# Performance work log

Measured on AMD Instinct MI355X. Metric: run time of the kernel, lower is better.

The kernel has to match this reference:

```python
import jax, jax.numpy as jnp
import numpy as np

HID, OUT = 128, 64
N_SOTU, N_TAXON = 500_000, 200_000
E_TT, E_TS, E_LBL = 200_000, 1_000_000, 500_000


def _sage(x_src, x_dst, src, dst, wl, bl, wr):
    """PyG SAGEConv (mean aggr): lin_l(mean of neighbor msgs) + lin_r(x_dst)."""
    n_dst = x_dst.shape[0]
    agg = jax.ops.segment_sum(x_src[src], dst, num_segments=n_dst)
    deg = jax.ops.segment_sum(jnp.ones(src.shape[0], x_src.dtype), dst, num_segments=n_dst)
    agg = agg / jnp.maximum(deg, 1.0)[:, None]
    return agg @ wl + bl + x_dst @ wr


def setup_inputs() -> dict:
    key = jax.random.key(0)
    ks = iter(jax.random.split(key, 40))

    def w(shape):
        fan_in = shape[0]
        return (jax.random.normal(next(ks), shape, jnp.float32) / np.sqrt(fan_in)).astype(jnp.float32)

    def ri(n, hi):
        return jax.random.randint(next(ks), (n,), 0, hi, dtype=jnp.int32)

    inp = {
        "sotu_ids": jnp.arange(N_SOTU, dtype=jnp.int32),
        "taxon_ids": jnp.arange(N_TAXON, dtype=jnp.int32),
        "ett_src": ri(E_TT, N_TAXON),
        "ett_dst": ri(E_TT, N_TAXON),
        "ets_src": ri(E_TS, N_TAXON),
        "ets_dst": ri(E_TS, N_SOTU),
        "elbl_row": ri(E_LBL, N_SOTU),
        "elbl_col": ri(E_LBL, N_TAXON),
        # embeddings
        "sotu_emb": jax.random.normal(next(ks), (N_SOTU, HID), jnp.float32),
        "taxon_emb": jax.random.normal(next(ks), (N_TAXON, HID), jnp.float32),
        # SOTU encoder: conv1 (taxon->taxon), conv2/3 (taxon->sotu), lin
        "s1_wl": w((HID, HID)), "s1_bl": jnp.zeros((HID,), jnp.float32), "s1_wr": w((HID, HID)),
        "s2_wl": w((HID, HID)), "s2_bl": jnp.zeros((HID,), jnp.float32), "s2_wr": w((HID, HID)),
        "s3_wl": w((HID, HID)), "s3_bl": jnp.zeros((HID,), jnp.float32), "s3_wr": w((HID, HID)),
        "sl_w": w((HID, OUT)), "sl_b": jnp.zeros((OUT,), jnp.float32),
        # Taxon encoder: conv1, conv2, lin
        "t1_wl": w((HID, HID)), "t1_bl": jnp.zeros((HID,), jnp.float32), "t1_wr": w((HID, HID)),
        "t2_wl": w((HID, HID)), "t2_bl": jnp.zeros((HID,), jnp.float32), "t2_wr": w((HID, HID)),
        "tl_w": w((HID, OUT)), "tl_b": jnp.zeros((OUT,), jnp.float32),
        # Edge decoder MLP
        "d1_w": w((2 * OUT, OUT)), "d1_b": jnp.zeros((OUT,), jnp.float32),
        "d2_w": w((OUT, 1)), "d2_b": jnp.zeros((1,), jnp.float32),
    }
    return inp


def reference(sotu_ids, taxon_ids, ett_src, ett_dst, ets_src, ets_dst,
              elbl_row, elbl_col, sotu_emb, taxon_emb,
              s1_wl, s1_bl, s1_wr, s2_wl, s2_bl, s2_wr, s3_wl, s3_bl, s3_wr,
              sl_w, sl_b, t1_wl, t1_bl, t1_wr, t2_wl, t2_bl, t2_wr, tl_w, tl_b,
              d1_w, d1_b, d2_w, d2_b):
    # embedding lookup
    x_sotu = sotu_emb[sotu_ids]          # [N_SOTU, HID]
    x_taxon = taxon_emb[taxon_ids]       # [N_TAXON, HID]
    # SOTU encoder
    taxon_x = jax.nn.relu(_sage(x_taxon, x_taxon, ett_src, ett_dst, s1_wl, s1_bl, s1_wr))
    sotu_x = jax.nn.relu(_sage(x_taxon, x_sotu, ets_src, ets_dst, s2_wl, s2_bl, s2_wr))
    sotu_x = jax.nn.relu(_sage(taxon_x, sotu_x, ets_src, ets_dst, s3_wl, s3_bl, s3_wr))
    z_sotu = sotu_x @ sl_w + sl_b        # [N_SOTU, OUT]
    # Taxon encoder
    tx = jax.nn.relu(_sage(x_taxon, x_taxon, ett_src, ett_dst, t1_wl, t1_bl, t1_wr))
    tx = jax.nn.relu(_sage(tx, tx, ett_src, ett_dst, t2_wl, t2_bl, t2_wr))
    z_taxon = tx @ tl_w + tl_b           # [N_TAXON, OUT]
    # Edge decoder: gather endpoints, fused MLP
    z = jnp.concatenate([z_sotu[elbl_row], z_taxon[elbl_col]], axis=-1)  # [E_LBL, 2*OUT]
    h = jax.nn.relu(z @ d1_w + d1_b)
    return (h @ d2_w + d2_b).reshape(-1)  # [E_LBL]
```

## Files before the change

### kernel.cpp

```cpp
#include <hip/hip_runtime.h>

#define HID 128
#define OUTD 64
#define N_SOTU 500000
#define N_TAXON 200000
#define E_TT 200000
#define E_TS 1000000
#define E_LBL 500000
#define HALF_S 250000
#define SCAN_TILE 2048

typedef short s16x8 __attribute__((ext_vector_type(8)));
typedef float f32x4 __attribute__((ext_vector_type(4)));

__device__ __forceinline__ unsigned short f2bf(float f) {
    unsigned u = __builtin_bit_cast(unsigned, f);
    u += 0x7FFFu + ((u >> 16) & 1u);
    return (unsigned short)(u >> 16);
}
__device__ __forceinline__ float bf2f(unsigned short h) {
    unsigned u = ((unsigned)h) << 16;
    return __builtin_bit_cast(float, u);
}

__global__ void hist_kernel(const int* __restrict__ dst, int n, int* __restrict__ rp) {
    int e = blockIdx.x * 256 + threadIdx.x;
    if (e < n) atomicAdd(&rp[dst[e]], 1);
}

__global__ __launch_bounds__(256) void scan1_kernel(int* __restrict__ a, int n, int* __restrict__ bsums) {
    __shared__ int tsum[256];
    const int t = threadIdx.x;
    const int base = blockIdx.x * SCAN_TILE + t * 8;
    int v[8]; int s = 0;
#pragma unroll
    for (int i = 0; i < 8; i++) {
        int x = (base + i < n) ? a[base + i] : 0;
        s += x; v[i] = s;
    }
    tsum[t] = s;
    __syncthreads();
    for (int off = 1; off < 256; off <<= 1) {
        int x = (t >= off) ? tsum[t - off] : 0;
        __syncthreads();
        tsum[t] += x;
        __syncthreads();
    }
    const int prev = (t > 0) ? tsum[t - 1] : 0;
#pragma unroll
    for (int i = 0; i < 8; i++)
        if (base + i < n) a[base + i] = v[i] + prev;
    if (t == 255) bsums[blockIdx.x] = tsum[255];
}

__global__ __launch_bounds__(256) void scan2_kernel(int* __restrict__ bsums, int nb) {
    __shared__ int tsum[256];
    const int t = threadIdx.x;
    tsum[t] = (t < nb) ? bsums[t] : 0;
    __syncthreads();
    for (int off = 1; off < 256; off <<= 1) {
        int x = (t >= off) ? tsum[t - off] : 0;
        __syncthreads();
        tsum[t] += x;
        __syncthreads();
    }
    if (t < nb) bsums[t] = tsum[t];
}

__global__ __launch_bounds__(256) void scan3_kernel(int* __restrict__ a, int n, const int* __restrict__ bsums) {
    const int b = blockIdx.x;
    if (b == 0) return;
    const int add = bsums[b - 1];
    const int base = b * SCAN_TILE + threadIdx.x * 8;
#pragma unroll
    for (int i = 0; i < 8; i++)
        if (base + i < n) a[base + i] += add;
}

__global__ void fill_kernel(const int* __restrict__ src, const int* __restrict__ dst, int n,
                            int* __restrict__ rp, int* __restrict__ sl) {
    int e = blockIdx.x * 256 + threadIdx.x;
    if (e < n) {
        int pos = atomicSub(&rp[dst[e]], 1) - 1;
        sl[pos] = src[e];
    }
}

__global__ __launch_bounds__(256) void gather_kernel(
    const float* __restrict__ xf, const unsigned short* __restrict__ xb,
    const int* __restrict__ xids,
    const int* __restrict__ rp, const int* __restrict__ sl,
    int n_dst_total, int n_edges, int lo, int rows,
    unsigned short* __restrict__ agg)
{
    const int g = blockIdx.x * 16 + (threadIdx.x >> 4);
    if (g >= rows) return;
    const int d = lo + g;
    const int l = threadIdx.x & 15;
    const int start = rp[d];
    const int end = (d + 1 < n_dst_total) ? rp[d + 1] : n_edges;
    float acc[8] = {0.f, 0.f, 0.f, 0.f, 0.f, 0.f, 0.f, 0.f};
    for (int j = start; j < end; ++j) {
        int s = sl[j];
        if (xids) s = xids[s];
        if (xf) {
            const float* p = xf + (size_t)s * HID + l * 8;
            float4 v0 = *(const float4*)p;
            float4 v1 = *(const float4*)(p + 4);
            acc[0] += v0.x; acc[1] += v0.y; acc[2] += v0.z; acc[3] += v0.w;
            acc[4] += v1.x; acc[5] += v1.y; acc[6] += v1.z; acc[7] += v1.w;
        } else {
            s16x8 b = *(const s16x8*)(xb + (size_t)s * HID + l * 8);
#pragma unroll
            for (int i = 0; i < 8; i++) acc[i] += bf2f((unsigned short)b[i]);
        }
    }
    const float inv = (end > start) ? 1.0f / (float)(end - start) : 0.0f;
    s16x8 o;
#pragma unroll
    for (int i = 0; i < 8; i++) o[i] = (short)f2bf(acc[i] * inv);
    *(s16x8*)(agg + (size_t)g * HID + l * 8) = o;
}

__device__ __forceinline__ int wt_idx(int n, int k) {
    return n * 256 + ((((k >> 3) ^ n) & 31) << 3) + (k & 7);
}

__global__ __launch_bounds__(256) void sage_kernel(
    int n_rows, int row0,
    const unsigned short* __restrict__ agg,
    const float* __restrict__ xf, const unsigned short* __restrict__ xb,
    const int* __restrict__ xids,
    const float* __restrict__ wl, const float* __restrict__ wr,
    const float* __restrict__ bl,
    unsigned short* __restrict__ out)
{
    __shared__ __align__(16) unsigned short WT[128 * 256];
    for (int idx = threadIdx.x; idx < 128 * 128; idx += 256) {
        int n = idx & 127, k = idx >> 7;
        WT[wt_idx(n, k)]       = f2bf(wl[idx]);
        WT[wt_idx(n, k + 128)] = f2bf(wr[idx]);
    }
    __syncthreads();
    const int lane = threadIdx.x & 63, wid = threadIdx.x >> 6;
    const int l16 = lane & 15, q = lane >> 4;
    const int n_tiles = n_rows >> 4;
    const int stride = gridDim.x * 4;
    for (int tile = blockIdx.x * 4 + wid; tile < n_tiles; tile += stride) {
        const int base = tile << 4;
        const int lrow = base + l16;
        const size_t xrow = xids ? (size_t)xids[lrow] : (size_t)(row0 + lrow);
        f32x4 acc[8] = {};
#pragma unroll
        for (int ks = 0; ks < 4; ks++) {
            s16x8 a = *(const s16x8*)(agg + (size_t)lrow * HID + ks * 32 + q * 8);
            const int kb = ks * 32 + q * 8;
#pragma unroll
            for (int nt = 0; nt < 8; nt++) {
                s16x8 b = *(const s16x8*)&WT[wt_idx(nt * 16 + l16, kb)];
                acc[nt] = __builtin_amdgcn_mfma_f32_16x16x32_bf16(a, b, acc[nt], 0, 0, 0);
            }
        }
#pragma unroll
        for (int ks = 0; ks < 4; ks++) {
            s16x8 a;
            if (xf) {
                const float* xp = xf + xrow * HID + ks * 32 + q * 8;
                float4 v0 = *(const float4*)xp;
                float4 v1 = *(const float4*)(xp + 4);
                a[0] = (short)f2bf(v0.x); a[1] = (short)f2bf(v0.y);
                a[2] = (short)f2bf(v0.z); a[3] = (short)f2bf(v0.w);
                a[4] = (short)f2bf(v1.x); a[5] = (short)f2bf(v1.y);
                a[6] = (short)f2bf(v1.z); a[7] = (short)f2bf(v1.w);
            } else {
                a = *(const s16x8*)(xb + xrow * HID + ks * 32 + q * 8);
            }
            const int kb = 128 + ks * 32 + q * 8;
#pragma unroll
            for (int nt = 0; nt < 8; nt++) {
                s16x8 b = *(const s16x8*)&WT[wt_idx(nt * 16 + l16, kb)];
                acc[nt] = __builtin_amdgcn_mfma_f32_16x16x32_bf16(a, b, acc[nt], 0, 0, 0);
            }
        }
#pragma unroll
        for (int nt = 0; nt < 8; nt++) {
            const int n = nt * 16 + l16;
            const float bv = bl[n];
#pragma unroll
            for (int i = 0; i < 4; i++) {
                float v = acc[nt][i] + bv;
                out[(size_t)(base + q * 4 + i) * HID + n] = f2bf(fmaxf(v, 0.0f));
            }
        }
    }
}

__global__ __launch_bounds__(256) void proj_kernel(
    int n_nodes, const unsigned short* __restrict__ x,
    const float* __restrict__ w, const float* __restrict__ bias, unsigned short* __restrict__ z)
{
    const int lane = threadIdx.x & 63, wid = threadIdx.x >> 6;
    const int l16 = lane & 15, q = lane >> 4;
    s16x8 bfr[4][4];
#pragma unroll
    for (int ks = 0; ks < 4; ks++)
#pragma unroll
        for (int nt = 0; nt < 4; nt++)
#pragma unroll
            for (int i = 0; i < 8; i++)
                bfr[ks][nt][i] = (short)f2bf(w[(ks * 32 + q * 8 + i) * OUTD + nt * 16 + l16]);
    const int n_tiles = n_nodes >> 4;
    const int stride = gridDim.x * 4;
    for (int tile = blockIdx.x * 4 + wid; tile < n_tiles; tile += stride) {
        const int base = tile << 4;
        const size_t mrow = (size_t)(base + l16);
        f32x4 acc[4] = {};
#pragma unroll
        for (int ks = 0; ks < 4; ks++) {
            s16x8 a = *(const s16x8*)(x + mrow * HID + ks * 32 + q * 8);
#pragma unroll
            for (int nt = 0; nt < 4; nt++)
                acc[nt] = __builtin_amdgcn_mfma_f32_16x16x32_bf16(a, bfr[ks][nt], acc[nt], 0, 0, 0);
        }
#pragma unroll
        for (int nt = 0; nt < 4; nt++) {
            const int n = nt * 16 + l16;
            const float bv = bias[n];
#pragma unroll
            for (int i = 0; i < 4; i++)
                z[(size_t)(base + q * 4 + i) * OUTD + n] = f2bf(acc[nt][i] + bv);
        }
    }
}

__global__ __launch_bounds__(256) void dec_kernel(
    const int* __restrict__ erow, const int* __restrict__ ecol,
    const unsigned short* __restrict__ zs, const unsigned short* __restrict__ zt,
    const float* __restrict__ w1, const float* __restrict__ b1,
    const float* __restrict__ w2, const float* __restrict__ b2,
    float* __restrict__ out)
{
    const int lane = threadIdx.x & 63, wid = threadIdx.x >> 6;
    const int l16 = lane & 15, q = lane >> 4;
    s16x8 bfr[4][4];
#pragma unroll
    for (int ks = 0; ks < 4; ks++)
#pragma unroll
        for (int nt = 0; nt < 4; nt++)
#pragma unroll
            for (int i = 0; i < 8; i++)
                bfr[ks][nt][i] = (short)f2bf(w1[(ks * 32 + q * 8 + i) * OUTD + nt * 16 + l16]);
    float b1v[4], w2v[4];
#pragma unroll
    for (int nt = 0; nt < 4; nt++) {
        b1v[nt] = b1[nt * 16 + l16];
        w2v[nt] = w2[nt * 16 + l16];
    }
    const float b2v = b2[0];
    const int n_tiles = E_LBL >> 4;
    for (int tile = blockIdx.x * 4 + wid; tile < n_tiles; tile += gridDim.x * 4) {
        const int em = tile * 16 + l16;
        const size_t r = (size_t)erow[em], c = (size_t)ecol[em];
        f32x4 acc[4] = {};
        s16x8 a0 = *(const s16x8*)(zs + r * OUTD + q * 8);
        s16x8 a1 = *(const s16x8*)(zs + r * OUTD + 32 + q * 8);
        s16x8 a2 = *(const s16x8*)(zt + c * OUTD + q * 8);
        s16x8 a3 = *(const s16x8*)(zt + c * OUTD + 32 + q * 8);
#pragma unroll
        for (int nt = 0; nt < 4; nt++) {
            acc[nt] = __builtin_amdgcn_mfma_f32_16x16x32_bf16(a0, bfr[0][nt], acc[nt], 0, 0, 0);
            acc[nt] = __builtin_amdgcn_mfma_f32_16x16x32_bf16(a1, bfr[1][nt], acc[nt], 0, 0, 0);
            acc[nt] = __builtin_amdgcn_mfma_f32_16x16x32_bf16(a2, bfr[2][nt], acc[nt], 0, 0, 0);
            acc[nt] = __builtin_amdgcn_mfma_f32_16x16x32_bf16(a3, bfr[3][nt], acc[nt], 0, 0, 0);
        }
        float s[4] = {0.0f, 0.0f, 0.0f, 0.0f};
#pragma unroll
        for (int nt = 0; nt < 4; nt++)
#pragma unroll
            for (int i = 0; i < 4; i++)
                s[i] += fmaxf(acc[nt][i] + b1v[nt], 0.0f) * w2v[nt];
#pragma unroll
        for (int off = 8; off >= 1; off >>= 1)
#pragma unroll
            for (int i = 0; i < 4; i++)
                s[i] += __shfl_down(s[i], off, 16);
        if (l16 == 0) {
#pragma unroll
            for (int i = 0; i < 4; i++)
                out[tile * 16 + q * 4 + i] = s[i] + b2v;
        }
    }
}

static void build_csr(const int* src, const int* dst, int n_edges, int n_dst,
                      int* rp, int* sl, int* bsums, hipStream_t stream) {
    hipMemsetAsync(rp, 0, (size_t)n_dst * 4, stream);
    hist_kernel<<<(n_edges + 255) / 256, 256, 0, stream>>>(dst, n_edges, rp);
    const int nb = (n_dst + SCAN_TILE - 1) / SCAN_TILE;
    scan1_kernel<<<nb, 256, 0, stream>>>(rp, n_dst, bsums);
    scan2_kernel<<<1, 256, 0, stream>>>(bsums, nb);
    scan3_kernel<<<nb, 256, 0, stream>>>(rp, n_dst, bsums);
    fill_kernel<<<(n_edges + 255) / 256, 256, 0, stream>>>(src, dst, n_edges, rp, sl);
}

extern "C" void kernel_launch(void* const* d_in, const int* in_sizes, int n_in,
                              void* d_out, int out_size, void* d_ws, size_t ws_size,
                              hipStream_t stream) {
    (void)in_sizes; (void)n_in; (void)out_size; (void)ws_size;
    const int* sotu_ids  = (const int*)d_in[0];
    const int* taxon_ids = (const int*)d_in[1];
    const int* ett_src   = (const int*)d_in[2];
    const int* ett_dst   = (const int*)d_in[3];
    const int* ets_src   = (const int*)d_in[4];
    const int* ets_dst   = (const int*)d_in[5];
    const int* elbl_row  = (const int*)d_in[6];
    const int* elbl_col  = (const int*)d_in[7];
    const float* sotu_emb  = (const float*)d_in[8];
    const float* taxon_emb = (const float*)d_in[9];
    const float* s1_wl = (const float*)d_in[10]; const float* s1_bl = (const float*)d_in[11]; const float* s1_wr = (const float*)d_in[12];
    const float* s2_wl = (const float*)d_in[13]; const float* s2_bl = (const float*)d_in[14]; const float* s2_wr = (const float*)d_in[15];
    const float* s3_wl = (const float*)d_in[16]; const float* s3_bl = (const float*)d_in[17]; const float* s3_wr = (const float*)d_in[18];
    const float* sl_w  = (const float*)d_in[19]; const float* sl_b  = (const float*)d_in[20];
    const float* t1_wl = (const float*)d_in[21]; const float* t1_bl = (const float*)d_in[22]; const float* t1_wr = (const float*)d_in[23];
    const float* t2_wl = (const float*)d_in[24]; const float* t2_bl = (const float*)d_in[25]; const float* t2_wr = (const float*)d_in[26];
    const float* tl_w  = (const float*)d_in[27]; const float* tl_b  = (const float*)d_in[28];
    const float* d1_w  = (const float*)d_in[29]; const float* d1_b  = (const float*)d_in[30];
    const float* d2_w  = (const float*)d_in[31]; const float* d2_b  = (const float*)d_in[32];
    float* out = (float*)d_out;

    char* ws = (char*)d_ws;
    size_t off = 0;
    auto alloc = [&](size_t bytes) { void* p = ws + off; off = (off + bytes + 255) & ~(size_t)255; return p; };
    unsigned short* agg     = (unsigned short*)alloc((size_t)HALF_S * HID * 2);
    unsigned short* taxon_x = (unsigned short*)alloc((size_t)N_TAXON * HID * 2);
    unsigned short* tx1     = (unsigned short*)alloc((size_t)N_TAXON * HID * 2);
    unsigned short* sotu_x  = (unsigned short*)alloc((size_t)N_SOTU * HID * 2);
    unsigned short* z_taxon = (unsigned short*)alloc((size_t)N_TAXON * OUTD * 2);
    int* rp_ts = (int*)alloc((size_t)N_SOTU * 4);
    int* sl_ts = (int*)alloc((size_t)E_TS * 4);
    int* rp_tt = (int*)alloc((size_t)N_TAXON * 4);
    int* sl_tt = (int*)alloc((size_t)E_TT * 4);
    int* bsums = (int*)alloc(256 * 4);
    unsigned short* z_sotu = agg;

    build_csr(ett_src, ett_dst, E_TT, N_TAXON, rp_tt, sl_tt, bsums, stream);
    build_csr(ets_src, ets_dst, E_TS, N_SOTU, rp_ts, sl_ts, bsums, stream);

    gather_kernel<<<(N_TAXON + 15) / 16, 256, 0, stream>>>(
        taxon_emb, nullptr, taxon_ids, rp_tt, sl_tt, N_TAXON, E_TT, 0, N_TAXON, agg);
    sage_kernel<<<512, 256, 0, stream>>>(N_TAXON, 0, agg, taxon_emb, nullptr, taxon_ids,
                                         s1_wl, s1_wr, s1_bl, taxon_x);
    sage_kernel<<<512, 256, 0, stream>>>(N_TAXON, 0, agg, taxon_emb, nullptr, taxon_ids,
                                         t1_wl, t1_wr, t1_bl, tx1);

    gather_kernel<<<(N_TAXON + 15) / 16, 256, 0, stream>>>(
        nullptr, tx1, nullptr, rp_tt, sl_tt, N_TAXON, E_TT, 0, N_TAXON, agg);
    sage_kernel<<<512, 256, 0, stream>>>(N_TAXON, 0, agg, nullptr, tx1, nullptr,
                                         t2_wl, t2_wr, t2_bl, tx1);
    proj_kernel<<<1024, 256, 0, stream>>>(N_TAXON, tx1, tl_w, tl_b, z_taxon);

    for (int h = 0; h < 2; ++h) {
        int lo = h * HALF_S;
        gather_kernel<<<(HALF_S + 15) / 16, 256, 0, stream>>>(
            taxon_emb, nullptr, taxon_ids, rp_ts, sl_ts, N_SOTU, E_TS, lo, HALF_S, agg);
        sage_kernel<<<512, 256, 0, stream>>>(HALF_S, lo, agg, sotu_emb, nullptr, sotu_ids + lo,
                                             s2_wl, s2_wr, s2_bl, sotu_x + (size_t)lo * HID);
    }
    for (int h = 0; h < 2; ++h) {
        int lo = h * HALF_S;
        gather_kernel<<<(HALF_S + 15) / 16, 256, 0, stream>>>(
            nullptr, taxon_x, nullptr, rp_ts, sl_ts, N_SOTU, E_TS, lo, HALF_S, agg);
        sage_kernel<<<512, 256, 0, stream>>>(HALF_S, lo, agg, nullptr, sotu_x, nullptr,
                                             s3_wl, s3_wr, s3_bl, sotu_x + (size_t)lo * HID);
    }
    proj_kernel<<<1024, 256, 0, stream>>>(N_SOTU, sotu_x, sl_w, sl_b, z_sotu);

    dec_kernel<<<1024, 256, 0, stream>>>(elbl_row, elbl_col, z_sotu, z_taxon,
                                         d1_w, d1_b, d2_w, d2_b, out);
}
```

Measured before the change: 1.629 ms.

## Fuse neighbor mean-aggregation into SAGE MFMA kernel via LDS staging

Removes the separate gather kernel and its global agg buffer by computing each 16-row tile's neighbor mean inside the SAGE kernel and staging it in swizzled LDS before the MFMA. Taxon embeddings are pre-converted to bf16 once so the gather reads half the bytes, and the SOTU layers run as single full launches instead of halves. This cuts global write/read traffic and launches, but adds LDS per block (possibly lower occupancy) and puts irregular gather latency in the same waves as the matmul. The conv1 self term now uses bf16 input converted from fp32, which matches the previous rounding. The only sync between the LDS write and the MFMA read is an lgkmcnt wait rather than a barrier, which relies on each wave's 64 lanes executing in lockstep.

```diff
diff --git a/kernel.cpp b/kernel.cpp
--- a/kernel.cpp
+++ b/kernel.cpp
@@ -7,7 +7,6 @@
 #define E_TT 200000
 #define E_TS 1000000
 #define E_LBL 500000
-#define HALF_S 250000
 #define SCAN_TILE 2048
 
 typedef short s16x8 __attribute__((ext_vector_type(8)));
@@ -86,49 +85,34 @@
     }
 }
 
-__global__ __launch_bounds__(256) void gather_kernel(
-    const float* __restrict__ xf, const unsigned short* __restrict__ xb,
-    const int* __restrict__ xids,
-    const int* __restrict__ rp, const int* __restrict__ sl,
-    int n_dst_total, int n_edges, int lo, int rows,
-    unsigned short* __restrict__ agg)
+__global__ __launch_bounds__(256) void cvt_kernel(
+    int n_rows, const float* __restrict__ xf, const int* __restrict__ ids,
+    unsigned short* __restrict__ o)
 {
-    const int g = blockIdx.x * 16 + (threadIdx.x >> 4);
-    if (g >= rows) return;
-    const int d = lo + g;
-    const int l = threadIdx.x & 15;
-    const int start = rp[d];
-    const int end = (d + 1 < n_dst_total) ? rp[d + 1] : n_edges;
-    float acc[8] = {0.f, 0.f, 0.f, 0.f, 0.f, 0.f, 0.f, 0.f};
-    for (int j = start; j < end; ++j) {
-        int s = sl[j];
-        if (xids) s = xids[s];
-        if (xf) {
-            const float* p = xf + (size_t)s * HID + l * 8;
-            float4 v0 = *(const float4*)p;
-            float4 v1 = *(const float4*)(p + 4);
-            acc[0] += v0.x; acc[1] += v0.y; acc[2] += v0.z; acc[3] += v0.w;
-            acc[4] += v1.x; acc[5] += v1.y; acc[6] += v1.z; acc[7] += v1.w;
-        } else {
-            s16x8 b = *(const s16x8*)(xb + (size_t)s * HID + l * 8);
-#pragma unroll
-            for (int i = 0; i < 8; i++) acc[i] += bf2f((unsigned short)b[i]);
-        }
-    }
-    const float inv = (end > start) ? 1.0f / (float)(end - start) : 0.0f;
-    s16x8 o;
-#pragma unroll
-    for (int i = 0; i < 8; i++) o[i] = (short)f2bf(acc[i] * inv);
-    *(s16x8*)(agg + (size_t)g * HID + l * 8) = o;
+    int idx = blockIdx.x * 256 + threadIdx.x;
+    if (idx >= n_rows * 16) return;
+    int r = idx >> 4, l = idx & 15;
+    int s = ids ? ids[r] : r;
+    const float* p = xf + (size_t)s * HID + l * 8;
+    float4 v0 = *(const float4*)p;
+    float4 v1 = *(const float4*)(p + 4);
+    s16x8 ov;
+    ov[0] = (short)f2bf(v0.x); ov[1] = (short)f2bf(v0.y);
+    ov[2] = (short)f2bf(v0.z); ov[3] = (short)f2bf(v0.w);
+    ov[4] = (short)f2bf(v1.x); ov[5] = (short)f2bf(v1.y);
+    ov[6] = (short)f2bf(v1.z); ov[7] = (short)f2bf(v1.w);
+    *(s16x8*)(o + (size_t)r * HID + l * 8) = ov;
 }
 
 __device__ __forceinline__ int wt_idx(int n, int k) {
     return n * 256 + ((((k >> 3) ^ n) & 31) << 3) + (k & 7);
 }
 
-__global__ __launch_bounds__(256) void sage_kernel(
+__global__ __launch_bounds__(256) void fsage_kernel(
     int n_rows, int row0,
-    const unsigned short* __restrict__ agg,
+    const unsigned short* __restrict__ gsrc,
+    const int* __restrict__ rp, const int* __restrict__ sl,
+    int n_dst_total, int n_edges,
     const float* __restrict__ xf, const unsigned short* __restrict__ xb,
     const int* __restrict__ xids,
     const float* __restrict__ wl, const float* __restrict__ wr,
@@ -136,6 +120,7 @@
     unsigned short* __restrict__ out)
 {
     __shared__ __align__(16) unsigned short WT[128 * 256];
+    __shared__ __align__(16) unsigned short AGG[4][16 * 128];
     for (int idx = threadIdx.x; idx < 128 * 128; idx += 256) {
         int n = idx & 127, k = idx >> 7;
         WT[wt_idx(n, k)]       = f2bf(wl[idx]);
@@ -148,16 +133,36 @@
     const int stride = gridDim.x * 4;
     for (int tile = blockIdx.x * 4 + wid; tile < n_tiles; tile += stride) {
         const int base = tile << 4;
+#pragma unroll
+        for (int it = 0; it < 4; ++it) {
+            const int lr = it * 4 + q;
+            const int d = row0 + base + lr;
+            const int start = rp[d];
+            const int end = (d + 1 < n_dst_total) ? rp[d + 1] : n_edges;
+            float acc[8] = {0.f, 0.f, 0.f, 0.f, 0.f, 0.f, 0.f, 0.f};
+            for (int j = start; j < end; ++j) {
+                const int s = sl[j];
+                s16x8 b = *(const s16x8*)(gsrc + (size_t)s * HID + l16 * 8);
+#pragma unroll
+                for (int i = 0; i < 8; i++) acc[i] += bf2f((unsigned short)b[i]);
+            }
+            const float inv = (end > start) ? 1.0f / (float)(end - start) : 0.0f;
+            s16x8 o;
+#pragma unroll
+            for (int i = 0; i < 8; i++) o[i] = (short)f2bf(acc[i] * inv);
+            *(s16x8*)&AGG[wid][lr * 128 + ((l16 * 8) ^ ((lr & 7) << 3))] = o;
+        }
+        asm volatile("s_waitcnt lgkmcnt(0)" ::: "memory");
         const int lrow = base + l16;
         const size_t xrow = xids ? (size_t)xids[lrow] : (size_t)(row0 + lrow);
         f32x4 acc[8] = {};
 #pragma unroll
         for (int ks = 0; ks < 4; ks++) {
-            s16x8 a = *(const s16x8*)(agg + (size_t)lrow * HID + ks * 32 + q * 8);
-            const int kb = ks * 32 + q * 8;
+            const int cu = ks * 32 + q * 8;
+            s16x8 a = *(const s16x8*)&AGG[wid][l16 * 128 + (cu ^ ((l16 & 7) << 3))];
 #pragma unroll
             for (int nt = 0; nt < 8; nt++) {
-                s16x8 b = *(const s16x8*)&WT[wt_idx(nt * 16 + l16, kb)];
+                s16x8 b = *(const s16x8*)&WT[wt_idx(nt * 16 + l16, cu)];
                 acc[nt] = __builtin_amdgcn_mfma_f32_16x16x32_bf16(a, b, acc[nt], 0, 0, 0);
             }
         }
@@ -331,9 +336,10 @@
     char* ws = (char*)d_ws;
     size_t off = 0;
     auto alloc = [&](size_t bytes) { void* p = ws + off; off = (off + bytes + 255) & ~(size_t)255; return p; };
-    unsigned short* agg     = (unsigned short*)alloc((size_t)HALF_S * HID * 2);
+    unsigned short* tb      = (unsigned short*)alloc((size_t)N_TAXON * HID * 2);
     unsigned short* taxon_x = (unsigned short*)alloc((size_t)N_TAXON * HID * 2);
     unsigned short* tx1     = (unsigned short*)alloc((size_t)N_TAXON * HID * 2);
+    unsigned short* tx2     = (unsigned short*)alloc((size_t)N_TAXON * HID * 2);
     unsigned short* sotu_x  = (unsigned short*)alloc((size_t)N_SOTU * HID * 2);
     unsigned short* z_taxon = (unsigned short*)alloc((size_t)N_TAXON * OUTD * 2);
     int* rp_ts = (int*)alloc((size_t)N_SOTU * 4);
@@ -341,38 +347,26 @@
     int* rp_tt = (int*)alloc((size_t)N_TAXON * 4);
     int* sl_tt = (int*)alloc((size_t)E_TT * 4);
     int* bsums = (int*)alloc(256 * 4);
-    unsigned short* z_sotu = agg;
+    unsigned short* z_sotu = tx1;
 
     build_csr(ett_src, ett_dst, E_TT, N_TAXON, rp_tt, sl_tt, bsums, stream);
     build_csr(ets_src, ets_dst, E_TS, N_SOTU, rp_ts, sl_ts, bsums, stream);
 
-    gather_kernel<<<(N_TAXON + 15) / 16, 256, 0, stream>>>(
-        taxon_emb, nullptr, taxon_ids, rp_tt, sl_tt, N_TAXON, E_TT, 0, N_TAXON, agg);
-    sage_kernel<<<512, 256, 0, stream>>>(N_TAXON, 0, agg, taxon_emb, nullptr, taxon_ids,
-                                         s1_wl, s1_wr, s1_bl, taxon_x);
-    sage_kernel<<<512, 256, 0, stream>>>(N_TAXON, 0, agg, taxon_emb, nullptr, taxon_ids,
-                                         t1_wl, t1_wr, t1_bl, tx1);
-
-    gather_kernel<<<(N_TAXON + 15) / 16, 256, 0, stream>>>(
-        nullptr, tx1, nullptr, rp_tt, sl_tt, N_TAXON, E_TT, 0, N_TAXON, agg);
-    sage_kernel<<<512, 256, 0, stream>>>(N_TAXON, 0, agg, nullptr, tx1, nullptr,
-                                         t2_wl, t2_wr, t2_bl, tx1);
-    proj_kernel<<<1024, 256, 0, stream>>>(N_TAXON, tx1, tl_w, tl_b, z_taxon);
-
-    for (int h = 0; h < 2; ++h) {
-        int lo = h * HALF_S;
-        gather_kernel<<<(HALF_S + 15) / 16, 256, 0, stream>>>(
-            taxon_emb, nullptr, taxon_ids, rp_ts, sl_ts, N_SOTU, E_TS, lo, HALF_S, agg);
-        sage_kernel<<<512, 256, 0, stream>>>(HALF_S, lo, agg, sotu_emb, nullptr, sotu_ids + lo,
-                                             s2_wl, s2_wr, s2_bl, sotu_x + (size_t)lo * HID);
-    }
-    for (int h = 0; h < 2; ++h) {
-        int lo = h * HALF_S;
-        gather_kernel<<<(HALF_S + 15) / 16, 256, 0, stream>>>(
-            nullptr, taxon_x, nullptr, rp_ts, sl_ts, N_SOTU, E_TS, lo, HALF_S, agg);
-        sage_kernel<<<512, 256, 0, stream>>>(HALF_S, lo, agg, nullptr, sotu_x, nullptr,
-                                             s3_wl, s3_wr, s3_bl, sotu_x + (size_t)lo * HID);
-    }
+    cvt_kernel<<<(N_TAXON * 16 + 255) / 256, 256, 0, stream>>>(N_TAXON, taxon_emb, taxon_ids, tb);
+
+    fsage_kernel<<<512, 256, 0, stream>>>(N_TAXON, 0, tb, rp_tt, sl_tt, N_TAXON, E_TT,
+                                          nullptr, tb, nullptr, s1_wl, s1_wr, s1_bl, taxon_x);
+    fsage_kernel<<<512, 256, 0, stream>>>(N_TAXON, 0, tb, rp_tt, sl_tt, N_TAXON, E_TT,
+                                          nullptr, tb, nullptr, t1_wl, t1_wr, t1_bl, tx1);
+
+    fsage_kernel<<<512, 256, 0, stream>>>(N_TAXON, 0, tx1, rp_tt, sl_tt, N_TAXON, E_TT,
+                                          nullptr, tx1, nullptr, t2_wl, t2_wr, t2_bl, tx2);
+    proj_kernel<<<1024, 256, 0, stream>>>(N_TAXON, tx2, tl_w, tl_b, z_taxon);
+
+    fsage_kernel<<<512, 256, 0, stream>>>(N_SOTU, 0, tb, rp_ts, sl_ts, N_SOTU, E_TS,
+                                          sotu_emb, nullptr, sotu_ids, s2_wl, s2_wr, s2_bl, sotu_x);
+    fsage_kernel<<<512, 256, 0, stream>>>(N_SOTU, 0, taxon_x, rp_ts, sl_ts, N_SOTU, E_TS,
+                                          nullptr, sotu_x, nullptr, s3_wl, s3_wr, s3_bl, sotu_x);
     proj_kernel<<<1024, 256, 0, stream>>>(N_SOTU, sotu_x, sl_w, sl_b, z_sotu);
 
     dec_kernel<<<1024, 256, 0, stream>>>(elbl_row, elbl_col, z_sotu, z_taxon,
```

Result: faster. 1.495 ms (-8.2%).
